# Kernel tuning notes

Hardware: AMD Instinct MI355X
Metric: run time of the kernel (lower is better)

## Reference

```python
import jax, jax.numpy as jnp
import numpy as np

DIM = 768
NUM_HEADS = 12
HEAD_DIM = DIM // NUM_HEADS
SCALE = HEAD_DIM ** -0.5


def setup_inputs() -> dict:
    key = jax.random.key(0)
    k1, k2, k3, k4 = jax.random.split(key, 4)
    B, N = 2, 4096
    x = jax.random.normal(k1, (B, N, DIM), dtype=jnp.float32)
    # qkv: nn.Linear(dim, 3*dim, bias=False)
    W_qkv = jax.random.normal(k2, (DIM, 3 * DIM), dtype=jnp.float32) * (DIM ** -0.5)
    # proj: nn.Linear(dim, dim) with bias
    W_proj = jax.random.normal(k3, (DIM, DIM), dtype=jnp.float32) * (DIM ** -0.5)
    b_proj = jax.random.normal(k4, (DIM,), dtype=jnp.float32) * 0.02
    return {"x": x, "W_qkv": W_qkv, "W_proj": W_proj, "b_proj": b_proj}


def reference(x, W_qkv, W_proj, b_proj):
    B, N, C = x.shape
    qkv = x @ W_qkv  # [B, N, 3C]
    qkv = qkv.reshape(B, N, 3, NUM_HEADS, HEAD_DIM)
    q = qkv[:, :, 0].transpose(0, 2, 1, 3)  # [B, H, N, D]
    k = qkv[:, :, 1].transpose(0, 2, 1, 3)
    v = qkv[:, :, 2].transpose(0, 2, 1, 3)
    attn = jnp.einsum('bhnd,bhmd->bhnm', q, k) * SCALE  # [B, H, N, N]
    attn = jax.nn.softmax(attn, axis=-1)
    out = jnp.einsum('bhnm,bhmd->bhnd', attn, v)  # [B, H, N, D]
    out = out.transpose(0, 2, 1, 3).reshape(B, N, C)
    return out @ W_proj + b_proj
```

## Files before the change

### kernel.cpp

```cpp
#include <hip/hip_runtime.h>
#include <stdint.h>

#define NBATCH 2
#define SEQ    4096
#define CDIM   768
#define NHEADS 12
#define HDIM   64
#define MTOK   (NBATCH*SEQ)
#define TC3    (3*CDIM)
#define QSCALE (0.125f * 1.4426950408889634f)
#define SMAX 12.0f

typedef unsigned short u16;
typedef __attribute__((ext_vector_type(8))) short bh8;
typedef __attribute__((ext_vector_type(4))) float f32x4;
typedef __attribute__((ext_vector_type(16))) float f32x16;
typedef __attribute__((ext_vector_type(4))) unsigned short us4;
typedef __attribute__((ext_vector_type(8))) unsigned short us8;

__device__ __forceinline__ u16 f2bf(float f) {
  union { float f; uint32_t u; } v; v.f = f;
  return (u16)((v.u + 0x7FFFu + ((v.u >> 16) & 1u)) >> 16);
}

__device__ __forceinline__ uint32_t cvt_pk_bf16(float a, float b) {
  uint32_t r;
  asm("v_cvt_pk_bf16_f32 %0, %1, %2" : "=v"(r) : "v"(a), "v"(b));
  return r;
}

#define GL_LDS16(src, dst) \
  __builtin_amdgcn_global_load_lds((const __attribute__((address_space(1))) void*)(src), \
                                   (__attribute__((address_space(3))) void*)(dst), 16, 0, 0)

__global__ void cast_x_kernel(const float* __restrict__ in, u16* __restrict__ out, int n4) {
  int i = blockIdx.x * blockDim.x + threadIdx.x;
  if (i >= n4) return;
  float4 v = ((const float4*)in)[i];
  us4 o;
  o[0] = f2bf(v.x); o[1] = f2bf(v.y); o[2] = f2bf(v.z); o[3] = f2bf(v.w);
  ((us4*)out)[i] = o;
}

__global__ void transpose_cast_kernel(const float* __restrict__ in, u16* __restrict__ out,
                                      int R, int C) {
  __shared__ float t[32][33];
  int c0 = blockIdx.x * 32, r0 = blockIdx.y * 32;
  int tx = threadIdx.x, ty = threadIdx.y;
#pragma unroll
  for (int i = 0; i < 4; ++i)
    t[ty + 8 * i][tx] = in[(r0 + ty + 8 * i) * C + c0 + tx];
  __syncthreads();
#pragma unroll
  for (int i = 0; i < 4; ++i)
    out[(c0 + ty + 8 * i) * R + r0 + tx] = f2bf(t[tx][ty + 8 * i]);
}

__global__ __launch_bounds__(256) void gemm_qkv_kernel(
    const u16* __restrict__ A, const u16* __restrict__ Bt,
    u16* __restrict__ Qs, u16* __restrict__ Kb, u16* __restrict__ Vt) {
  __shared__ __align__(16) u16 As[128 * 32];
  __shared__ __align__(16) u16 Bs[128 * 32];
  int blk = blockIdx.x;
  int bm = blk / 18, bn = blk % 18;
  int m0 = bm * 128, n0 = bn * 128;
  int tid = threadIdx.x;
  int wv = tid >> 6, ln = tid & 63;
  int wr = wv >> 1, wc = wv & 1;

  f32x4 acc[4][4];
#pragma unroll
  for (int i = 0; i < 4; ++i)
#pragma unroll
    for (int j = 0; j < 4; ++j) acc[i][j] = (f32x4){0.f, 0.f, 0.f, 0.f};

  const char* Ab = (const char*)(A + m0 * CDIM);
  const char* Bb = (const char*)(Bt + n0 * CDIM);

  for (int kt = 0; kt < CDIM / 32; ++kt) {
#pragma unroll
    for (int i = 0; i < 2; ++i) {
      int idx = i * 256 + tid;
      int r = idx >> 2, c = idx & 3;
      int cs = c ^ ((r >> 1) & 3);
      GL_LDS16(Ab + r * (CDIM * 2) + kt * 64 + cs * 16, (char*)As + idx * 16);
      GL_LDS16(Bb + r * (CDIM * 2) + kt * 64 + cs * 16, (char*)Bs + idx * 16);
    }
    __syncthreads();

    bh8 af[4];
#pragma unroll
    for (int mi = 0; mi < 4; ++mi) {
      int r = 64 * wr + 16 * mi + (ln & 15);
      int cs = (ln >> 4) ^ ((r >> 1) & 3);
      af[mi] = *(const bh8*)((const char*)As + r * 64 + cs * 16);
    }
#pragma unroll
    for (int nj = 0; nj < 4; ++nj) {
      int r = 64 * wc + 16 * nj + (ln & 15);
      int cs = (ln >> 4) ^ ((r >> 1) & 3);
      bh8 bf = *(const bh8*)((const char*)Bs + r * 64 + cs * 16);
#pragma unroll
      for (int mi = 0; mi < 4; ++mi)
        acc[mi][nj] = __builtin_amdgcn_mfma_f32_16x16x32_bf16(af[mi], bf, acc[mi][nj], 0, 0, 0);
    }
    __syncthreads();
  }

  int b = m0 >> 12;
#pragma unroll
  for (int nj = 0; nj < 4; ++nj) {
    int nb = n0 + 64 * wc + 16 * nj;
    int which = nb / CDIM;
    int rem = nb % CDIM;
    int h = rem / 64;
    int d = (rem % 64) + (ln & 15);
#pragma unroll
    for (int mi = 0; mi < 4; ++mi) {
      int t0 = (m0 & 4095) + 64 * wr + 16 * mi + ((ln >> 4) << 2);
      f32x4 v = acc[mi][nj];
      if (which == 0) {
#pragma unroll
        for (int q = 0; q < 4; ++q)
          Qs[((b * 12 + h) * 4096 + t0 + q) * 64 + d] = f2bf(v[q] * QSCALE);
      } else if (which == 1) {
#pragma unroll
        for (int q = 0; q < 4; ++q)
          Kb[((b * 12 + h) * 4096 + t0 + q) * 64 + d] = f2bf(v[q]);
      } else {
        us4 o;
#pragma unroll
        for (int q = 0; q < 4; ++q) o[q] = f2bf(v[q]);
        *(us4*)(Vt + ((b * 12 + h) * 64 + d) * 4096 + t0) = o;
      }
    }
  }
}

__device__ __forceinline__ void softmax_pack(
    const f32x16& s, float& lsum, bh8& pf_lo, bh8& pf_hi) {
  float p[16];
#pragma unroll
  for (int e = 0; e < 16; ++e) { p[e] = __builtin_amdgcn_exp2f(s[e]); lsum += p[e]; }
  unsigned int W[8];
#pragma unroll
  for (int g = 0; g < 4; ++g) {
    W[2 * g]     = cvt_pk_bf16(p[4 * g],     p[4 * g + 1]);
    W[2 * g + 1] = cvt_pk_bf16(p[4 * g + 2], p[4 * g + 3]);
  }
  unsigned int a0 = W[0], a1 = W[2], b0 = W[1], b1 = W[3];
  asm("v_permlane32_swap_b32 %0, %1" : "+v"(a0), "+v"(a1));
  asm("v_permlane32_swap_b32 %0, %1" : "+v"(b0), "+v"(b1));
  unsigned int c0 = W[4], c1 = W[6], d0 = W[5], d1 = W[7];
  asm("v_permlane32_swap_b32 %0, %1" : "+v"(c0), "+v"(c1));
  asm("v_permlane32_swap_b32 %0, %1" : "+v"(d0), "+v"(d1));
  union { unsigned int u[4]; bh8 v; } u0, u1;
  u0.u[0] = a0; u0.u[1] = b0; u0.u[2] = a1; u0.u[3] = b1;
  u1.u[0] = c0; u1.u[1] = d0; u1.u[2] = c1; u1.u[3] = d1;
  pf_lo = u0.v; pf_hi = u1.v;
}

__device__ __forceinline__ void attn_tile64(
    const char* kb, const char* vb, const bh8* qf,
    f32x16* od, float& lsum, int q31, int h, int x7) {
  f32x16 s0, s1;
#pragma unroll
  for (int e = 0; e < 16; ++e) { s0[e] = -SMAX; s1[e] = -SMAX; }
  __builtin_amdgcn_s_setprio(1);
#pragma unroll
  for (int ks = 0; ks < 4; ++ks) {
    int cs = ((2 * ks + h) ^ x7) * 16;
    bh8 k0 = *(const bh8*)(kb + q31 * 128 + cs);
    s0 = __builtin_amdgcn_mfma_f32_32x32x16_bf16(k0, qf[ks], s0, 0, 0, 0);
    bh8 k1 = *(const bh8*)(kb + (32 + q31) * 128 + cs);
    s1 = __builtin_amdgcn_mfma_f32_32x32x16_bf16(k1, qf[ks], s1, 0, 0, 0);
  }
  __builtin_amdgcn_s_setprio(0);

  bh8 pf[4];
  softmax_pack(s0, lsum, pf[0], pf[1]);
  softmax_pack(s1, lsum, pf[2], pf[3]);

  __builtin_amdgcn_s_setprio(1);
#pragma unroll
  for (int m = 0; m < 4; ++m) {
    int cs = ((2 * m + h) ^ x7) * 16;
    bh8 v0 = *(const bh8*)(vb + q31 * 128 + cs);
    od[0] = __builtin_amdgcn_mfma_f32_32x32x16_bf16(v0, pf[m], od[0], 0, 0, 0);
    bh8 v1 = *(const bh8*)(vb + (32 + q31) * 128 + cs);
    od[1] = __builtin_amdgcn_mfma_f32_32x32x16_bf16(v1, pf[m], od[1], 0, 0, 0);
  }
  __builtin_amdgcn_s_setprio(0);
}

__global__ __launch_bounds__(256, 3) void attn_kernel(
    const u16* __restrict__ Qs, const u16* __restrict__ Kb,
    const u16* __restrict__ Vt,
    float* __restrict__ Op0, float* __restrict__ Op1, float* __restrict__ Lp) {
  __shared__ __align__(16) u16 Ks[2 * 64 * 64];
  __shared__ __align__(16) u16 Vs[2 * 64 * 64];
  int blk = blockIdx.x;
  int xcd = blk & 7, ii = blk >> 3;
  int bh = xcd + 8 * (ii >> 6);
  int rem = ii & 63;
  int h2 = rem >> 5;
  int qt = rem & 31;
  int tid = threadIdx.x, wv = tid >> 6, ln = tid & 63;
  int q31 = ln & 31, h = ln >> 5, x7 = ln & 7;

  const u16* qrow = Qs + (bh * 4096 + qt * 128 + wv * 32 + q31) * 64;
  bh8 qf[4];
#pragma unroll
  for (int ks = 0; ks < 4; ++ks)
    qf[ks] = *(const bh8*)(qrow + 16 * ks + 8 * h);

  f32x16 od[2];
#pragma unroll
  for (int e = 0; e < 16; ++e) { od[0][e] = 0.f; od[1][e] = 0.f; }
  float lsum = 0.f;

  const char* Kt0 = (const char*)(Kb + bh * 4096 * 64) + h2 * 2048 * 128;
  const char* Vt0 = (const char*)(Vt + bh * 64 * 4096) + h2 * 4096;

  int r0 = tid >> 3, c0 = tid & 7, cs0 = (c0 ^ (r0 & 7)) * 16;
  const char* ksrcA = Kt0 + r0 * 128 + cs0;
  const char* ksrcB = Kt0 + (r0 + 32) * 128 + cs0;
  const char* vsrcA = Vt0 + r0 * 8192 + cs0;
  const char* vsrcB = Vt0 + (r0 + 32) * 8192 + cs0;
  char* kd = (char*)Ks + tid * 16;
  char* vd = (char*)Vs + tid * 16;

  GL_LDS16(ksrcA, kd); GL_LDS16(ksrcB, kd + 4096);
  GL_LDS16(vsrcA, vd); GL_LDS16(vsrcB, vd + 4096);
  __syncthreads();

  const char* kb0 = (const char*)Ks; const char* kb1 = kb0 + 8192;
  const char* vb0 = (const char*)Vs; const char* vb1 = vb0 + 8192;

  for (int t = 0; t < 16; ++t) {
    GL_LDS16(ksrcA + (2 * t + 1) * 8192, kd + 8192);
    GL_LDS16(ksrcB + (2 * t + 1) * 8192, kd + 12288);
    GL_LDS16(vsrcA + (2 * t + 1) * 128, vd + 8192);
    GL_LDS16(vsrcB + (2 * t + 1) * 128, vd + 12288);
    attn_tile64(kb0, vb0, qf, od, lsum, q31, h, x7);
    __syncthreads();
    if (t < 15) {
      GL_LDS16(ksrcA + (2 * t + 2) * 8192, kd);
      GL_LDS16(ksrcB + (2 * t + 2) * 8192, kd + 4096);
      GL_LDS16(vsrcA + (2 * t + 2) * 128, vd);
      GL_LDS16(vsrcB + (2 * t + 2) * 128, vd + 4096);
    }
    attn_tile64(kb1, vb1, qf, od, lsum, q31, h, x7);
    __syncthreads();
  }

  float l = lsum + __shfl_xor(lsum, 32);

  int b = bh / 12, hd = bh % 12;
  int token = qt * 128 + wv * 32 + q31;
  float* Op = h2 ? Op1 : Op0;
  float* obase = Op + (size_t)(b * 4096 + token) * 768 + hd * 64;
#pragma unroll
  for (int db = 0; db < 2; ++db)
#pragma unroll
    for (int g = 0; g < 4; ++g) {
      float4 w;
      w.x = od[db][4 * g + 0]; w.y = od[db][4 * g + 1];
      w.z = od[db][4 * g + 2]; w.w = od[db][4 * g + 3];
      *(float4*)(obase + 32 * db + 8 * g + 4 * h) = w;
    }
  if (h == 0) Lp[h2 * (24 * 4096) + bh * 4096 + token] = l;
}

__global__ __launch_bounds__(256) void combine_kernel(
    const float* __restrict__ Op0, const float* __restrict__ Op1,
    const float* __restrict__ Lp, u16* __restrict__ attn) {
  int idx = blockIdx.x * 256 + threadIdx.x;
  int i8 = idx * 8;
  int row = i8 / 768;
  int c = i8 - row * 768;
  int hd = c >> 6;
  int b = row >> 12, n = row & 4095;
  int li = (b * 12 + hd) * 4096 + n;
  float inv = 1.0f / (Lp[li] + Lp[24 * 4096 + li]);
  float4 a0 = *(const float4*)(Op0 + i8);
  float4 a1 = *(const float4*)(Op0 + i8 + 4);
  float4 b0 = *(const float4*)(Op1 + i8);
  float4 b1 = *(const float4*)(Op1 + i8 + 4);
  us8 w;
  w[0] = f2bf((a0.x + b0.x) * inv); w[1] = f2bf((a0.y + b0.y) * inv);
  w[2] = f2bf((a0.z + b0.z) * inv); w[3] = f2bf((a0.w + b0.w) * inv);
  w[4] = f2bf((a1.x + b1.x) * inv); w[5] = f2bf((a1.y + b1.y) * inv);
  w[6] = f2bf((a1.z + b1.z) * inv); w[7] = f2bf((a1.w + b1.w) * inv);
  *(us8*)(attn + i8) = w;
}

__global__ __launch_bounds__(256) void gemm_proj_kernel(
    const u16* __restrict__ A, const u16* __restrict__ Bt,
    const float* __restrict__ bias, float* __restrict__ out) {
  __shared__ __align__(16) u16 As[128 * 32];
  __shared__ __align__(16) u16 Bs[128 * 32];
  int blk = blockIdx.x;
  int bm = blk / 6, bn = blk % 6;
  int m0 = bm * 128, n0 = bn * 128;
  int tid = threadIdx.x;
  int wv = tid >> 6, ln = tid & 63;
  int wr = wv >> 1, wc = wv & 1;

  f32x4 acc[4][4];
#pragma unroll
  for (int i = 0; i < 4; ++i)
#pragma unroll
    for (int j = 0; j < 4; ++j) acc[i][j] = (f32x4){0.f, 0.f, 0.f, 0.f};

  const char* Ab = (const char*)(A + m0 * CDIM);
  const char* Bb = (const char*)(Bt + n0 * CDIM);

  for (int kt = 0; kt < CDIM / 32; ++kt) {
#pragma unroll
    for (int i = 0; i < 2; ++i) {
      int idx = i * 256 + tid;
      int r = idx >> 2, c = idx & 3;
      int cs = c ^ ((r >> 1) & 3);
      GL_LDS16(Ab + r * (CDIM * 2) + kt * 64 + cs * 16, (char*)As + idx * 16);
      GL_LDS16(Bb + r * (CDIM * 2) + kt * 64 + cs * 16, (char*)Bs + idx * 16);
    }
    __syncthreads();

    bh8 af[4];
#pragma unroll
    for (int mi = 0; mi < 4; ++mi) {
      int r = 64 * wr + 16 * mi + (ln & 15);
      int cs = (ln >> 4) ^ ((r >> 1) & 3);
      af[mi] = *(const bh8*)((const char*)As + r * 64 + cs * 16);
    }
#pragma unroll
    for (int nj = 0; nj < 4; ++nj) {
      int r = 64 * wc + 16 * nj + (ln & 15);
      int cs = (ln >> 4) ^ ((r >> 1) & 3);
      bh8 bf = *(const bh8*)((const char*)Bs + r * 64 + cs * 16);
#pragma unroll
      for (int mi = 0; mi < 4; ++mi)
        acc[mi][nj] = __builtin_amdgcn_mfma_f32_16x16x32_bf16(af[mi], bf, acc[mi][nj], 0, 0, 0);
    }
    __syncthreads();
  }

#pragma unroll
  for (int nj = 0; nj < 4; ++nj) {
    int col = n0 + 64 * wc + 16 * nj + (ln & 15);
    float bv = bias[col];
#pragma unroll
    for (int mi = 0; mi < 4; ++mi) {
      int row = m0 + 64 * wr + 16 * mi + ((ln >> 4) << 2);
#pragma unroll
      for (int q = 0; q < 4; ++q)
        out[(row + q) * CDIM + col] = acc[mi][nj][q] + bv;
    }
  }
}

extern "C" void kernel_launch(void* const* d_in, const int* in_sizes, int n_in,
                              void* d_out, int out_size, void* d_ws, size_t ws_size,
                              hipStream_t stream) {
  const float* x     = (const float*)d_in[0];
  const float* Wqkv  = (const float*)d_in[1];
  const float* Wproj = (const float*)d_in[2];
  const float* bias  = (const float*)d_in[3];
  float* out = (float*)d_out;

  u16* xb   = (u16*)d_ws;
  u16* Wqt  = xb + MTOK * CDIM;
  u16* Wpt  = Wqt + TC3 * CDIM;
  u16* Qs   = Wpt + CDIM * CDIM;
  u16* Kb   = Qs + 24 * 4096 * 64;
  u16* Vt   = Kb + 24 * 4096 * 64;
  u16* attn = Vt + 24 * 64 * 4096;
  float* Op1 = (float*)(attn + MTOK * CDIM);
  float* Lp  = Op1 + MTOK * CDIM;
  float* Op0 = out;

  cast_x_kernel<<<6144, 256, 0, stream>>>(x, xb, (MTOK * CDIM) / 4);
  transpose_cast_kernel<<<dim3(TC3 / 32, CDIM / 32), dim3(32, 8), 0, stream>>>(Wqkv, Wqt, CDIM, TC3);
  transpose_cast_kernel<<<dim3(CDIM / 32, CDIM / 32), dim3(32, 8), 0, stream>>>(Wproj, Wpt, CDIM, CDIM);
  gemm_qkv_kernel<<<(MTOK / 128) * (TC3 / 128), 256, 0, stream>>>(xb, Wqt, Qs, Kb, Vt);
  attn_kernel<<<1536, 256, 0, stream>>>(Qs, Kb, Vt, Op0, Op1, Lp);
  combine_kernel<<<(MTOK * CDIM) / (256 * 8), 256, 0, stream>>>(Op0, Op1, Lp, attn);
  gemm_proj_kernel<<<(MTOK / 128) * (CDIM / 128), 256, 0, stream>>>(attn, Wpt, bias, out);
}
```

Before: 211.8 us.

## Process 64 queries per wave to reuse K/V LDS fragments across two query sets

Each wave now handles two 32-row query groups, loading K fragments once into registers and reusing each V fragment for both groups, with tiles split into two 32-key halves. The grid is halved accordingly. This cuts LDS read traffic per MFMA. In exchange, accumulator register pressure doubles, which may reduce occupancy or cause spills, and fewer blocks lower the available parallelism.

Measured after the change: 519.1 us. 145% more time.

```diff
diff --git a/kernel.cpp b/kernel.cpp
--- a/kernel.cpp
+++ b/kernel.cpp
@@ -160,35 +160,41 @@
   pf_lo = u0.v; pf_hi = u1.v;
 }
 
-__device__ __forceinline__ void attn_tile64(
-    const char* kb, const char* vb, const bh8* qf,
-    f32x16* od, float& lsum, int q31, int h, int x7) {
+__device__ __forceinline__ void attn_half(
+    const char* kb, const char* vb, const bh8* qf0, const bh8* qf1,
+    f32x16* od, float& ls0, float& ls1, int kblk,
+    int q31, int h, int x7) {
+  const char* krow = kb + (kblk * 32 + q31) * 128;
+  bh8 kf[4];
+#pragma unroll
+  for (int ks = 0; ks < 4; ++ks)
+    kf[ks] = *(const bh8*)(krow + ((2 * ks + h) ^ x7) * 16);
+
   f32x16 s0, s1;
 #pragma unroll
   for (int e = 0; e < 16; ++e) { s0[e] = -SMAX; s1[e] = -SMAX; }
   __builtin_amdgcn_s_setprio(1);
 #pragma unroll
   for (int ks = 0; ks < 4; ++ks) {
-    int cs = ((2 * ks + h) ^ x7) * 16;
-    bh8 k0 = *(const bh8*)(kb + q31 * 128 + cs);
-    s0 = __builtin_amdgcn_mfma_f32_32x32x16_bf16(k0, qf[ks], s0, 0, 0, 0);
-    bh8 k1 = *(const bh8*)(kb + (32 + q31) * 128 + cs);
-    s1 = __builtin_amdgcn_mfma_f32_32x32x16_bf16(k1, qf[ks], s1, 0, 0, 0);
+    s0 = __builtin_amdgcn_mfma_f32_32x32x16_bf16(kf[ks], qf0[ks], s0, 0, 0, 0);
+    s1 = __builtin_amdgcn_mfma_f32_32x32x16_bf16(kf[ks], qf1[ks], s1, 0, 0, 0);
   }
   __builtin_amdgcn_s_setprio(0);
 
-  bh8 pf[4];
-  softmax_pack(s0, lsum, pf[0], pf[1]);
-  softmax_pack(s1, lsum, pf[2], pf[3]);
+  bh8 p0[2], p1[2];
+  softmax_pack(s0, ls0, p0[0], p0[1]);
+  softmax_pack(s1, ls1, p1[0], p1[1]);
 
   __builtin_amdgcn_s_setprio(1);
 #pragma unroll
-  for (int m = 0; m < 4; ++m) {
-    int cs = ((2 * m + h) ^ x7) * 16;
+  for (int mm = 0; mm < 2; ++mm) {
+    int cs = ((2 * (2 * kblk + mm) + h) ^ x7) * 16;
     bh8 v0 = *(const bh8*)(vb + q31 * 128 + cs);
-    od[0] = __builtin_amdgcn_mfma_f32_32x32x16_bf16(v0, pf[m], od[0], 0, 0, 0);
+    od[0] = __builtin_amdgcn_mfma_f32_32x32x16_bf16(v0, p0[mm], od[0], 0, 0, 0);
+    od[1] = __builtin_amdgcn_mfma_f32_32x32x16_bf16(v0, p1[mm], od[1], 0, 0, 0);
     bh8 v1 = *(const bh8*)(vb + (32 + q31) * 128 + cs);
-    od[1] = __builtin_amdgcn_mfma_f32_32x32x16_bf16(v1, pf[m], od[1], 0, 0, 0);
+    od[2] = __builtin_amdgcn_mfma_f32_32x32x16_bf16(v1, p0[mm], od[2], 0, 0, 0);
+    od[3] = __builtin_amdgcn_mfma_f32_32x32x16_bf16(v1, p1[mm], od[3], 0, 0, 0);
   }
   __builtin_amdgcn_s_setprio(0);
 }
@@ -201,23 +207,27 @@
   __shared__ __align__(16) u16 Vs[2 * 64 * 64];
   int blk = blockIdx.x;
   int xcd = blk & 7, ii = blk >> 3;
-  int bh = xcd + 8 * (ii >> 6);
-  int rem = ii & 63;
-  int h2 = rem >> 5;
-  int qt = rem & 31;
+  int bh = xcd + 8 * (ii >> 5);
+  int rem = ii & 31;
+  int h2 = rem >> 4;
+  int qt = rem & 15;
   int tid = threadIdx.x, wv = tid >> 6, ln = tid & 63;
   int q31 = ln & 31, h = ln >> 5, x7 = ln & 7;
 
-  const u16* qrow = Qs + (bh * 4096 + qt * 128 + wv * 32 + q31) * 64;
-  bh8 qf[4];
-#pragma unroll
-  for (int ks = 0; ks < 4; ++ks)
-    qf[ks] = *(const bh8*)(qrow + 16 * ks + 8 * h);
-
-  f32x16 od[2];
-#pragma unroll
-  for (int e = 0; e < 16; ++e) { od[0][e] = 0.f; od[1][e] = 0.f; }
-  float lsum = 0.f;
+  const u16* qbase = Qs + (bh * 4096 + qt * 256 + wv * 64 + q31) * 64;
+  bh8 qf0[4], qf1[4];
+#pragma unroll
+  for (int ks = 0; ks < 4; ++ks) {
+    qf0[ks] = *(const bh8*)(qbase + 16 * ks + 8 * h);
+    qf1[ks] = *(const bh8*)(qbase + 32 * 64 + 16 * ks + 8 * h);
+  }
+
+  f32x16 od[4];
+#pragma unroll
+  for (int i = 0; i < 4; ++i)
+#pragma unroll
+    for (int e = 0; e < 16; ++e) od[i][e] = 0.f;
+  float ls0 = 0.f, ls1 = 0.f;
 
   const char* Kt0 = (const char*)(Kb + bh * 4096 * 64) + h2 * 2048 * 128;
   const char* Vt0 = (const char*)(Vt + bh * 64 * 4096) + h2 * 4096;
@@ -242,7 +252,9 @@
     GL_LDS16(ksrcB + (2 * t + 1) * 8192, kd + 12288);
     GL_LDS16(vsrcA + (2 * t + 1) * 128, vd + 8192);
     GL_LDS16(vsrcB + (2 * t + 1) * 128, vd + 12288);
-    attn_tile64(kb0, vb0, qf, od, lsum, q31, h, x7);
+    attn_half(kb0, vb0, qf0, qf1, od, ls0, ls1, 0, q31, h, x7);
+    __builtin_amdgcn_sched_barrier(0);
+    attn_half(kb0, vb0, qf0, qf1, od, ls0, ls1, 1, q31, h, x7);
     __syncthreads();
     if (t < 15) {
       GL_LDS16(ksrcA + (2 * t + 2) * 8192, kd);
@@ -250,26 +262,36 @@
       GL_LDS16(vsrcA + (2 * t + 2) * 128, vd);
       GL_LDS16(vsrcB + (2 * t + 2) * 128, vd + 4096);
     }
-    attn_tile64(kb1, vb1, qf, od, lsum, q31, h, x7);
-    __syncthreads();
-  }
-
-  float l = lsum + __shfl_xor(lsum, 32);
+    attn_half(kb1, vb1, qf0, qf1, od, ls0, ls1, 0, q31, h, x7);
+    __builtin_amdgcn_sched_barrier(0);
+    attn_half(kb1, vb1, qf0, qf1, od, ls0, ls1, 1, q31, h, x7);
+    __syncthreads();
+  }
+
+  float l0 = ls0 + __shfl_xor(ls0, 32);
+  float l1 = ls1 + __shfl_xor(ls1, 32);
 
   int b = bh / 12, hd = bh % 12;
-  int token = qt * 128 + wv * 32 + q31;
+  int tok0 = qt * 256 + wv * 64 + q31;
   float* Op = h2 ? Op1 : Op0;
-  float* obase = Op + (size_t)(b * 4096 + token) * 768 + hd * 64;
+  float* ob0 = Op + (size_t)(b * 4096 + tok0) * 768 + hd * 64;
+  float* ob1 = ob0 + 32 * 768;
 #pragma unroll
   for (int db = 0; db < 2; ++db)
 #pragma unroll
     for (int g = 0; g < 4; ++g) {
-      float4 w;
-      w.x = od[db][4 * g + 0]; w.y = od[db][4 * g + 1];
-      w.z = od[db][4 * g + 2]; w.w = od[db][4 * g + 3];
-      *(float4*)(obase + 32 * db + 8 * g + 4 * h) = w;
-    }
-  if (h == 0) Lp[h2 * (24 * 4096) + bh * 4096 + token] = l;
+      float4 w0, w1;
+      w0.x = od[2 * db][4 * g + 0]; w0.y = od[2 * db][4 * g + 1];
+      w0.z = od[2 * db][4 * g + 2]; w0.w = od[2 * db][4 * g + 3];
+      w1.x = od[2 * db + 1][4 * g + 0]; w1.y = od[2 * db + 1][4 * g + 1];
+      w1.z = od[2 * db + 1][4 * g + 2]; w1.w = od[2 * db + 1][4 * g + 3];
+      *(float4*)(ob0 + 32 * db + 8 * g + 4 * h) = w0;
+      *(float4*)(ob1 + 32 * db + 8 * g + 4 * h) = w1;
+    }
+  if (h == 0) {
+    Lp[h2 * (24 * 4096) + bh * 4096 + tok0] = l0;
+    Lp[h2 * (24 * 4096) + bh * 4096 + tok0 + 32] = l1;
+  }
 }
 
 __global__ __launch_bounds__(256) void combine_kernel(
@@ -384,7 +406,7 @@
   transpose_cast_kernel<<<dim3(TC3 / 32, CDIM / 32), dim3(32, 8), 0, stream>>>(Wqkv, Wqt, CDIM, TC3);
   transpose_cast_kernel<<<dim3(CDIM / 32, CDIM / 32), dim3(32, 8), 0, stream>>>(Wproj, Wpt, CDIM, CDIM);
   gemm_qkv_kernel<<<(MTOK / 128) * (TC3 / 128), 256, 0, stream>>>(xb, Wqt, Qs, Kb, Vt);
-  attn_kernel<<<1536, 256, 0, stream>>>(Qs, Kb, Vt, Op0, Op1, Lp);
+  attn_kernel<<<768, 256, 0, stream>>>(Qs, Kb, Vt, Op0, Op1, Lp);
   combine_kernel<<<(MTOK * CDIM) / (256 * 8), 256, 0, stream>>>(Op0, Op1, Lp, attn);
   gemm_proj_kernel<<<(MTOK / 128) * (CDIM / 128), 256, 0, stream>>>(attn, Wpt, bias, out);
 }
```
